# Kernel optimization log

Measured on AMD Instinct MI355X. Metric: run time of the kernel, lower is better.

## Reference

```python
import jax, jax.numpy as jnp
import numpy as np

N_NODES = 50000
N_EDGES = 800000
NFEAT, NHID, NCLASS = 512, 64, 40


def setup_inputs() -> dict:
    key = jax.random.key(0)
    ks = jax.random.split(key, 10)
    x = jax.random.normal(ks[0], (N_NODES, NFEAT), dtype=jnp.float32)
    edge_weight = jax.random.uniform(ks[1], (N_EDGES,), dtype=jnp.float32)
    W1 = jax.random.normal(ks[2], (NFEAT, NHID), dtype=jnp.float32) / np.sqrt(NFEAT)
    b1 = jnp.zeros((NHID,), dtype=jnp.float32)
    W2 = jax.random.normal(ks[3], (NHID, NHID), dtype=jnp.float32) / np.sqrt(NHID)
    b2 = jnp.zeros((NHID,), dtype=jnp.float32)
    W3 = jax.random.normal(ks[4], (NHID, NCLASS), dtype=jnp.float32) / np.sqrt(NHID)
    b3 = jnp.zeros((NCLASS,), dtype=jnp.float32)
    row = jax.random.randint(ks[5], (N_EDGES,), 0, N_NODES, dtype=jnp.int32)
    col = jax.random.randint(ks[6], (N_EDGES,), 0, N_NODES, dtype=jnp.int32)
    return {"x": x, "edge_weight": edge_weight, "W1": W1, "b1": b1,
            "W2": W2, "b2": b2, "W3": W3, "b3": b3, "row": row, "col": col}


def _gcn_layer(h, W, b, row, col, ew):
    # support = h @ W + b ; out = spmm(adj, support)
    support = h @ W + b                      # [N, dout]
    msg = support[col] * ew[:, None]         # gather + scale, [E, dout]
    return jax.ops.segment_sum(msg, row, num_segments=N_NODES)


def reference(x, edge_weight, W1, b1, W2, b2, W3, b3, row, col):
    h = jax.nn.relu(_gcn_layer(x, W1, b1, row, col, edge_weight))
    # dropout: eval mode -> identity
    h = _gcn_layer(h, W2, b2, row, col, edge_weight)
    h = _gcn_layer(h, W3, b3, row, col, edge_weight)
    return jax.nn.log_softmax(h, axis=1)
```

## Files before the change

kernel.cpp:

```cpp
#include <hip/hip_runtime.h>
#include <hip/hip_bf16.h>

#define NNODES 50000
#define NEDGES 800000
#define NFEAT  512
#define NHID   64
#define NCLASS 40

#define CAP 48
#define CNTSTRIDE 16
#define GEMM1_BLOCKS ((NNODES + 63) / 64)

#define WINDOWS 98
#define FILLGRID (WINDOWS * 40)
#define SLICES 392
#define SLICE_EDGES ((NEDGES + SLICES - 1) / SLICES)
#define PART_NODES (NNODES / 8)

typedef __attribute__((ext_vector_type(8))) short short8;
typedef __attribute__((ext_vector_type(4))) float floatx4;

static __device__ __forceinline__ unsigned short f2bf(float f) {
    union { float f; unsigned u; } v; v.f = f;
    const unsigned r = v.u + 0x7fffu + ((v.u >> 16) & 1u);
    return (unsigned short)(r >> 16);
}
static __device__ __forceinline__ float bf2f(unsigned u) {
    union { unsigned u; float f; } v; v.u = u << 16;
    return v.f;
}

template<int NCB, int NVALID>
static __device__ __forceinline__ void convW_body(
    const float* __restrict__ W, unsigned short* __restrict__ wb, int idx) {
    const int lane = idx & 63;
    const int cb   = (idx >> 6) % NCB;
    const int kb   = idx / (64 * NCB);
    const int q = lane >> 4, m = lane & 15;
    const int c = cb * 16 + m;
    short8 v;
    #pragma unroll
    for (int j = 0; j < 8; ++j)
        v[j] = (c < NVALID)
             ? (short)f2bf(W[(size_t)(kb * 32 + q * 8 + j) * NVALID + c])
             : (short)0;
    *(short8*)(wb + (size_t)idx * 8) = v;
}

__global__ __launch_bounds__(256) void conv_kernel(
    const float* __restrict__ W1, unsigned short* __restrict__ wb1,
    const float* __restrict__ W2, unsigned short* __restrict__ wb2,
    const float* __restrict__ W3, unsigned short* __restrict__ wb3,
    int4* __restrict__ cnt4) {
    const int blk = blockIdx.x;
    const int tid = threadIdx.x;
    if (blk < 16) {
        convW_body<4, 64>(W1, wb1, blk * 256 + tid);
    } else if (blk < 18) {
        convW_body<4, 64>(W2, wb2, (blk - 16) * 256 + tid);
    } else if (blk < 20) {
        const int idx = (blk - 18) * 256 + tid;
        if (idx < 2 * 3 * 64) convW_body<3, 40>(W3, wb3, idx);
    } else {
        const int i = (blk - 20) * 256 + tid;
        if (i < NNODES * CNTSTRIDE / 4) cnt4[i] = make_int4(0, 0, 0, 0);
    }
}

__global__ __launch_bounds__(256) void bucket_gemm1_kernel(
    const int* __restrict__ row, const int* __restrict__ col,
    const float* __restrict__ ew, int* __restrict__ cnt,
    unsigned* __restrict__ bucket,
    const float* __restrict__ x, const unsigned short* __restrict__ wb,
    const float* __restrict__ b, unsigned short* __restrict__ outb) {
    const int blk = blockIdx.x;
    const int tid = threadIdx.x;

    if (blk % 5 != 0) {
        const int q = blk & 7;
        const int w = blk / 40;
        const int j_self = ((blk % 40) - q) >> 3;
        const int j0 = (5 - ((2 * q) % 5)) % 5;
        const int t = j_self - (j_self > j0 ? 1 : 0);
        const int slice = w * 4 + t;
        const int ebase = slice * SLICE_EDGES;
        const int eend  = (ebase + SLICE_EDGES < NEDGES) ? ebase + SLICE_EDGES : NEDGES;
        const int lo = q * PART_NODES;
        const int hi = lo + PART_NODES;
        for (int e = ebase + tid; e < eend; e += 256) {
            const int rr = row[e];
            if (rr >= lo && rr < hi) {
                const int pos = atomicAdd(&cnt[rr * CNTSTRIDE], 1);
                if (pos < CAP)
                    bucket[(size_t)rr * CAP + pos] =
                        (unsigned)col[e] | ((unsigned)f2bf(ew[e]) << 16);
            }
        }
        return;
    }

    const int g = blk / 5;
    if (g >= GEMM1_BLOCKS) return;
    const int lane = tid & 63;
    const int wid  = tid >> 6;
    const int q = lane >> 4, m = lane & 15;

    const int rowbase = g * 64 + wid * 16;
    int rload = rowbase + m;
    if (rload >= NNODES) rload = NNODES - 1;
    const float* xp = x + (size_t)rload * NFEAT + q * 8;

    floatx4 acc[4];
    #pragma unroll
    for (int cb = 0; cb < 4; ++cb) acc[cb] = (floatx4)0.f;

    for (int kb = 0; kb < 16; ++kb) {
        const float4 a0 = *(const float4*)(xp + kb * 32);
        const float4 a1 = *(const float4*)(xp + kb * 32 + 4);
        short8 afrag;
        afrag[0] = (short)f2bf(a0.x); afrag[1] = (short)f2bf(a0.y);
        afrag[2] = (short)f2bf(a0.z); afrag[3] = (short)f2bf(a0.w);
        afrag[4] = (short)f2bf(a1.x); afrag[5] = (short)f2bf(a1.y);
        afrag[6] = (short)f2bf(a1.z); afrag[7] = (short)f2bf(a1.w);

        const unsigned short* wp = wb + ((size_t)(kb * 4) * 64 + lane) * 8;
        #pragma unroll
        for (int cb = 0; cb < 4; ++cb) {
            const short8 bfrag = *(const short8*)(wp + (size_t)cb * 64 * 8);
            acc[cb] = __builtin_amdgcn_mfma_f32_16x16x32_bf16(
                afrag, bfrag, acc[cb], 0, 0, 0);
        }
    }

    const int orow = rowbase + q * 4;
    #pragma unroll
    for (int cb = 0; cb < 4; ++cb) {
        const int c = cb * 16 + m;
        const float bias = b[c];
        #pragma unroll
        for (int i = 0; i < 4; ++i) {
            const int rr2 = orow + i;
            if (rr2 < NNODES)
                outb[(size_t)rr2 * NHID + c] = f2bf(acc[cb][i] + bias);
        }
    }
}

template<bool RELU, int NCB, int NOUT>
__global__ __launch_bounds__(256) void spmm_gemm_kernel(
    const unsigned short* __restrict__ supb, const unsigned* __restrict__ bucket,
    const int* __restrict__ cnt, const unsigned short* __restrict__ wb,
    const float* __restrict__ bias, unsigned short* __restrict__ outb) {
    __shared__ unsigned short ht[4 * 72];

    const int tid  = threadIdx.x;
    const int wid  = tid >> 6;
    const int lane = tid & 63;
    const int half = lane >> 5;
    const int fp   = lane & 31;
    const int n    = blockIdx.x * 4 + wid;

    float a0 = 0.f, a1 = 0.f;
    if (n < NNODES) {
        int deg = cnt[n * CNTSTRIDE];
        if (deg > CAP) deg = CAP;
        const unsigned* ep = bucket + (size_t)n * CAP;
        for (int i = half; i < deg; i += 16) {
            unsigned eb[8], vb[8];
            #pragma unroll
            for (int j = 0; j < 8; ++j) {
                const int idx = i + 2 * j;
                eb[j] = (idx < deg) ? ep[idx] : 0u;
            }
            #pragma unroll
            for (int j = 0; j < 8; ++j)
                vb[j] = *(const unsigned*)(supb + (size_t)(eb[j] & 0xffffu) * NHID + fp * 2);
            #pragma unroll
            for (int j = 0; j < 8; ++j) {
                const float w = bf2f(eb[j] >> 16);
                a0 += w * bf2f(vb[j] & 0xffffu);
                a1 += w * bf2f(vb[j] >> 16);
            }
        }
    }
    a0 += __shfl_xor(a0, 32);
    a1 += __shfl_xor(a1, 32);
    if (RELU) { a0 = fmaxf(a0, 0.f); a1 = fmaxf(a1, 0.f); }
    if (half == 0)
        *(unsigned*)&ht[wid * 72 + fp * 2] =
            (unsigned)f2bf(a0) | ((unsigned)f2bf(a1) << 16);
    __syncthreads();

    if (wid != 0) return;
    const int q = lane >> 4, m = lane & 15;
    const unsigned short* hp = &ht[(m & 3) * 72 + q * 8];

    floatx4 acc[NCB];
    #pragma unroll
    for (int cb = 0; cb < NCB; ++cb) acc[cb] = (floatx4)0.f;

    #pragma unroll
    for (int kb = 0; kb < 2; ++kb) {
        const short8 afrag = *(const short8*)(hp + kb * 32);
        const unsigned short* wp = wb + ((size_t)(kb * NCB) * 64 + lane) * 8;
        #pragma unroll
        for (int cb = 0; cb < NCB; ++cb) {
            const short8 bfrag = *(const short8*)(wp + (size_t)cb * 64 * 8);
            acc[cb] = __builtin_amdgcn_mfma_f32_16x16x32_bf16(
                afrag, bfrag, acc[cb], 0, 0, 0);
        }
    }

    if (q != 0) return;
    #pragma unroll
    for (int cb = 0; cb < NCB; ++cb) {
        const int c = cb * 16 + m;
        if (c >= NOUT) continue;
        const float bv = bias[c];
        #pragma unroll
        for (int i = 0; i < 4; ++i) {
            const int r = blockIdx.x * 4 + i;
            if (r < NNODES)
                outb[(size_t)r * NOUT + c] = f2bf(acc[cb][i] + bv);
        }
    }
}

__global__ __launch_bounds__(256) void spmm_bf40_lsm_kernel(
    const unsigned short* __restrict__ supb, const unsigned* __restrict__ bucket,
    const int* __restrict__ cnt, float* __restrict__ out) {
    const int f = threadIdx.x & 63;
    const int n = blockIdx.x * 4 + (threadIdx.x >> 6);
    if (n >= NNODES) return;
    int deg = cnt[n * CNTSTRIDE];
    if (deg > CAP) deg = CAP;
    const unsigned* ep = bucket + (size_t)n * CAP;
    float acc = 0.f;
    if (f < NCLASS) {
        for (int i = 0; i < deg; i += 8) {
            unsigned eb[8]; float vb[8];
            #pragma unroll
            for (int j = 0; j < 8; ++j) {
                const int idx = i + j;
                eb[j] = (idx < deg) ? ep[idx] : 0u;
            }
            #pragma unroll
            for (int j = 0; j < 8; ++j)
                vb[j] = bf2f(supb[(size_t)(eb[j] & 0xffffu) * NCLASS + f]);
            #pragma unroll
            for (int j = 0; j < 8; ++j)
                acc += vb[j] * bf2f(eb[j] >> 16);
        }
    }
    float m = (f < NCLASS) ? acc : -1e30f;
    #pragma unroll
    for (int o = 32; o > 0; o >>= 1) m = fmaxf(m, __shfl_xor(m, o));
    float ex = (f < NCLASS) ? __expf(acc - m) : 0.f;
    #pragma unroll
    for (int o = 32; o > 0; o >>= 1) ex += __shfl_xor(ex, o);
    const float ls = __logf(ex) + m;
    if (f < NCLASS) out[(size_t)n * NCLASS + f] = acc - ls;
}

extern "C" void kernel_launch(void* const* d_in, const int* in_sizes, int n_in,
                              void* d_out, int out_size, void* d_ws, size_t ws_size,
                              hipStream_t stream) {
    const float* x  = (const float*)d_in[0];
    const float* ew = (const float*)d_in[1];
    const float* W1 = (const float*)d_in[2];
    const float* b1 = (const float*)d_in[3];
    const float* W2 = (const float*)d_in[4];
    const float* b2 = (const float*)d_in[5];
    const float* W3 = (const float*)d_in[6];
    const float* b3 = (const float*)d_in[7];
    const int* row  = (const int*)d_in[8];
    const int* col  = (const int*)d_in[9];
    float* out = (float*)d_out;

    const size_t n64 = (size_t)NNODES * NHID;
    const size_t n40 = (size_t)NNODES * NCLASS;
    unsigned* bucket = (unsigned*)d_ws;
    int* cnt = (int*)(bucket + (size_t)NNODES * CAP);
    unsigned short* S1 = (unsigned short*)(cnt + (size_t)NNODES * CNTSTRIDE);
    unsigned short* S2 = S1 + n64;
    unsigned short* S3 = S2 + n64;
    unsigned short* wb1 = S3 + n40;
    unsigned short* wb2 = wb1 + 16 * 4 * 64 * 8;
    unsigned short* wb3 = wb2 + 2 * 4 * 64 * 8;

    const int nodeBlocks = (NNODES + 3) / 4;

    conv_kernel<<<820, 256, 0, stream>>>(W1, wb1, W2, wb2, W3, wb3, (int4*)cnt);

    bucket_gemm1_kernel<<<FILLGRID, 256, 0, stream>>>(
        row, col, ew, cnt, bucket, x, wb1, b1, S1);

    spmm_gemm_kernel<true, 4, 64><<<nodeBlocks, 256, 0, stream>>>(
        S1, bucket, cnt, wb2, b2, S2);

    spmm_gemm_kernel<false, 3, 40><<<nodeBlocks, 256, 0, stream>>>(
        S2, bucket, cnt, wb3, b3, S3);

    spmm_bf40_lsm_kernel<<<nodeBlocks, 256, 0, stream>>>(S3, bucket, cnt, out);
}
```

Before: 310.8 us.

## Pre-bin edges by destination partition before bucket fill

Adds a binning pass that groups each edge, packed as (row, col|bf16 weight), into one of eight node-partition bins using per-block shared counters and a global atomic offset. The bucket-fill blocks then read only their own partition's bin instead of scanning every edge and discarding seven eighths of them. This removes the eightfold redundant reads of row, col and ew in the fused fill/GEMM kernel. In exchange it adds a kernel launch, an extra write and read of about 6.4 MB of binned edges, and a fixed bin capacity that silently drops edges if a partition overflows.

```diff
diff --git a/kernel.cpp b/kernel.cpp
--- a/kernel.cpp
+++ b/kernel.cpp
@@ -10,12 +10,11 @@
 #define CAP 48
 #define CNTSTRIDE 16
 #define GEMM1_BLOCKS ((NNODES + 63) / 64)
-
+#define PART_NODES (NNODES / 8)
+#define BINCAP 110000
 #define WINDOWS 98
 #define FILLGRID (WINDOWS * 40)
 #define SLICES 392
-#define SLICE_EDGES ((NEDGES + SLICES - 1) / SLICES)
-#define PART_NODES (NNODES / 8)
 
 typedef __attribute__((ext_vector_type(8))) short short8;
 typedef __attribute__((ext_vector_type(4))) float floatx4;
@@ -51,7 +50,7 @@
     const float* __restrict__ W1, unsigned short* __restrict__ wb1,
     const float* __restrict__ W2, unsigned short* __restrict__ wb2,
     const float* __restrict__ W3, unsigned short* __restrict__ wb3,
-    int4* __restrict__ cnt4) {
+    int4* __restrict__ cnt4, int* __restrict__ gcnt) {
     const int blk = blockIdx.x;
     const int tid = threadIdx.x;
     if (blk < 16) {
@@ -62,15 +61,44 @@
         const int idx = (blk - 18) * 256 + tid;
         if (idx < 2 * 3 * 64) convW_body<3, 40>(W3, wb3, idx);
     } else {
+        if (blk == 20 && tid < 8) gcnt[tid] = 0;
         const int i = (blk - 20) * 256 + tid;
         if (i < NNODES * CNTSTRIDE / 4) cnt4[i] = make_int4(0, 0, 0, 0);
     }
 }
 
+__global__ __launch_bounds__(256) void binpass_kernel(
+    const int* __restrict__ row, const int* __restrict__ col,
+    const float* __restrict__ ew, int* __restrict__ gcnt,
+    int2* __restrict__ binned) {
+    __shared__ int hcnt[8];
+    __shared__ int gbase[8];
+    const int tid = threadIdx.x;
+    const int e = blockIdx.x * 256 + tid;
+    if (tid < 8) hcnt[tid] = 0;
+    __syncthreads();
+    int rr = 0, p = 0, rank = 0;
+    unsigned entry = 0;
+    const bool valid = e < NEDGES;
+    if (valid) {
+        rr = row[e];
+        entry = (unsigned)col[e] | ((unsigned)f2bf(ew[e]) << 16);
+        p = rr / PART_NODES;
+        rank = atomicAdd(&hcnt[p], 1);
+    }
+    __syncthreads();
+    if (tid < 8) gbase[tid] = atomicAdd(&gcnt[tid], hcnt[tid]);
+    __syncthreads();
+    if (valid) {
+        const int idx = gbase[p] + rank;
+        if (idx < BINCAP)
+            binned[(size_t)p * BINCAP + idx] = make_int2(rr, (int)entry);
+    }
+}
+
 __global__ __launch_bounds__(256) void bucket_gemm1_kernel(
-    const int* __restrict__ row, const int* __restrict__ col,
-    const float* __restrict__ ew, int* __restrict__ cnt,
-    unsigned* __restrict__ bucket,
+    const int2* __restrict__ binned, const int* __restrict__ gcnt,
+    int* __restrict__ cnt, unsigned* __restrict__ bucket,
     const float* __restrict__ x, const unsigned short* __restrict__ wb,
     const float* __restrict__ b, unsigned short* __restrict__ outb) {
     const int blk = blockIdx.x;
@@ -83,18 +111,18 @@
         const int j0 = (5 - ((2 * q) % 5)) % 5;
         const int t = j_self - (j_self > j0 ? 1 : 0);
         const int slice = w * 4 + t;
-        const int ebase = slice * SLICE_EDGES;
-        const int eend  = (ebase + SLICE_EDGES < NEDGES) ? ebase + SLICE_EDGES : NEDGES;
-        const int lo = q * PART_NODES;
-        const int hi = lo + PART_NODES;
-        for (int e = ebase + tid; e < eend; e += 256) {
-            const int rr = row[e];
-            if (rr >= lo && rr < hi) {
-                const int pos = atomicAdd(&cnt[rr * CNTSTRIDE], 1);
-                if (pos < CAP)
-                    bucket[(size_t)rr * CAP + pos] =
-                        (unsigned)col[e] | ((unsigned)f2bf(ew[e]) << 16);
-            }
+        int cq = gcnt[q];
+        if (cq > BINCAP) cq = BINCAP;
+        const int chunk = (cq + SLICES - 1) / SLICES;
+        const int base = slice * chunk;
+        int end = base + chunk;
+        if (end > cq) end = cq;
+        const int2* src = binned + (size_t)q * BINCAP;
+        for (int i = base + tid; i < end; i += 256) {
+            const int2 ed = src[i];
+            const int pos = atomicAdd(&cnt[ed.x * CNTSTRIDE], 1);
+            if (pos < CAP)
+                bucket[(size_t)ed.x * CAP + pos] = (unsigned)ed.y;
         }
         return;
     }
@@ -281,7 +309,9 @@
     const size_t n40 = (size_t)NNODES * NCLASS;
     unsigned* bucket = (unsigned*)d_ws;
     int* cnt = (int*)(bucket + (size_t)NNODES * CAP);
-    unsigned short* S1 = (unsigned short*)(cnt + (size_t)NNODES * CNTSTRIDE);
+    int2* binned = (int2*)(cnt + (size_t)NNODES * CNTSTRIDE);
+    int* gcnt = (int*)(binned + (size_t)8 * BINCAP);
+    unsigned short* S1 = (unsigned short*)(gcnt + 8);
     unsigned short* S2 = S1 + n64;
     unsigned short* S3 = S2 + n64;
     unsigned short* wb1 = S3 + n40;
@@ -290,10 +320,14 @@
 
     const int nodeBlocks = (NNODES + 3) / 4;
 
-    conv_kernel<<<820, 256, 0, stream>>>(W1, wb1, W2, wb2, W3, wb3, (int4*)cnt);
+    conv_kernel<<<820, 256, 0, stream>>>(W1, wb1, W2, wb2, W3, wb3,
+                                         (int4*)cnt, gcnt);
+
+    binpass_kernel<<<(NEDGES + 255) / 256, 256, 0, stream>>>(
+        row, col, ew, gcnt, binned);
 
     bucket_gemm1_kernel<<<FILLGRID, 256, 0, stream>>>(
-        row, col, ew, cnt, bucket, x, wb1, b1, S1);
+        binned, gcnt, cnt, bucket, x, wb1, b1, S1);
 
     spmm_gemm_kernel<true, 4, 64><<<nodeBlocks, 256, 0, stream>>>(
         S1, bucket, cnt, wb2, b2, S2);
```

New measurement: 342.1 us. 10.1% more time.
